# Kernel optimization log

Measured on AMD Instinct MI355X. Metric: run time of the kernel, lower is better.

## Reference

```python
import jax, jax.numpy as jnp
import numpy as np

N_NODES = 10000

def setup_inputs() -> dict:
    key = jax.random.key(0)
    k1, k2, k3, k4, k5 = jax.random.split(key, 5)
    n_edges = 640000
    d_in = 128
    d_out = 128
    x = jax.random.normal(k1, (N_NODES, d_in), dtype=jnp.float32)
    src = jax.random.randint(k2, (n_edges,), 0, N_NODES, dtype=jnp.int32)
    dst = jax.random.randint(k3, (n_edges,), 0, N_NODES, dtype=jnp.int32)
    W = jax.random.normal(k4, (d_in, d_out), dtype=jnp.float32) * (1.0 / np.sqrt(d_in))
    b = jax.random.normal(k5, (d_out,), dtype=jnp.float32) * 0.01
    return {"x": x, "src": src, "dst": dst, "W": W, "b": b}

def reference(x, src, dst, W, b):
    # copy_src + sum reduce: for each edge, send x[src]; each node sums incoming msgs
    msgs = x[src]  # [E, d_in] gather
    h = jax.ops.segment_sum(msgs, dst, num_segments=N_NODES)  # [N, d_in] scatter-add
    # dropout p=0.0 -> identity; linear + relu
    out = jax.nn.relu(h @ W + b)  # [N, d_out]
    return out
```

## Files before the change

kernel.cpp:

```cpp
#include <hip/hip_runtime.h>

#define N_NODES 10000
#define D 128
#define N_EDGES 640000
#define SHARDS 8
#define CPAD 16
#define BCAP 32
#define GEMM_BLOCKS 313
#define FILL_BLOCKS 625

__device__ __forceinline__ unsigned short f2bf(float f) {
  unsigned int u = __float_as_uint(f);
  unsigned int r = (u + 0x7fffu + ((u >> 16) & 1u)) >> 16;
  return (unsigned short)r;
}
__device__ __forceinline__ float bf2f(unsigned short s) {
  return __uint_as_float((unsigned int)s << 16);
}

__device__ __forceinline__ int cidx(int d, int sh) {
  return ((d << 3) | sh) << 4;
}

__global__ __launch_bounds__(256) void gcn_fused_kernel(
    const float* __restrict__ x, const float* __restrict__ W,
    unsigned short* __restrict__ xw,
    const int* __restrict__ src, const int* __restrict__ dst,
    int* __restrict__ counts, unsigned short* __restrict__ srcs_pad) {
  __shared__ unsigned short Wl[D * D];

  if (blockIdx.x < FILL_BLOCKS) {
    const int e4 = (blockIdx.x * 256 + threadIdx.x) * 4;
    const int sh = blockIdx.x & (SHARDS - 1);
    const int4 d4 = *(const int4*)(dst + e4);
    const int4 s4 = *(const int4*)(src + e4);

    int r0 = atomicAdd(&counts[cidx(d4.x, sh)], 1);
    int r1 = atomicAdd(&counts[cidx(d4.y, sh)], 1);
    int r2 = atomicAdd(&counts[cidx(d4.z, sh)], 1);
    int r3 = atomicAdd(&counts[cidx(d4.w, sh)], 1);
    if (r0 < BCAP) srcs_pad[((size_t)d4.x * SHARDS + sh) * BCAP + r0] = (unsigned short)s4.x;
    if (r1 < BCAP) srcs_pad[((size_t)d4.y * SHARDS + sh) * BCAP + r1] = (unsigned short)s4.y;
    if (r2 < BCAP) srcs_pad[((size_t)d4.z * SHARDS + sh) * BCAP + r2] = (unsigned short)s4.z;
    if (r3 < BCAP) srcs_pad[((size_t)d4.w * SHARDS + sh) * BCAP + r3] = (unsigned short)s4.w;
    return;
  }

  for (int i = threadIdx.x; i < D * D; i += 256) Wl[i] = f2bf(W[i]);
  __syncthreads();

  const int bid = blockIdx.x - FILL_BLOCKS;
  const int c0 = (threadIdx.x & 31) * 4;
  const int r0 = bid * 32 + (threadIdx.x >> 5) * 4;
  if (r0 >= N_NODES) return;

  float4 acc0 = {0, 0, 0, 0}, acc1 = acc0, acc2 = acc0, acc3 = acc0;
  const float* x0 = x + (size_t)r0 * D;

#define GEMM_STEP(J, HC)                                              \
  {                                                                   \
    ushort4 wu = *(const ushort4*)&Wl[(k4 + J) * D + c0];             \
    float wx = bf2f(wu.x), wy = bf2f(wu.y);                           \
    float wz = bf2f(wu.z), ww = bf2f(wu.w);                           \
    acc0.x = fmaf(hv0.HC, wx, acc0.x);                                \
    acc0.y = fmaf(hv0.HC, wy, acc0.y);                                \
    acc0.z = fmaf(hv0.HC, wz, acc0.z);                                \
    acc0.w = fmaf(hv0.HC, ww, acc0.w);                                \
    acc1.x = fmaf(hv1.HC, wx, acc1.x);                                \
    acc1.y = fmaf(hv1.HC, wy, acc1.y);                                \
    acc1.z = fmaf(hv1.HC, wz, acc1.z);                                \
    acc1.w = fmaf(hv1.HC, ww, acc1.w);                                \
    acc2.x = fmaf(hv2.HC, wx, acc2.x);                                \
    acc2.y = fmaf(hv2.HC, wy, acc2.y);                                \
    acc2.z = fmaf(hv2.HC, wz, acc2.z);                                \
    acc2.w = fmaf(hv2.HC, ww, acc2.w);                                \
    acc3.x = fmaf(hv3.HC, wx, acc3.x);                                \
    acc3.y = fmaf(hv3.HC, wy, acc3.y);                                \
    acc3.z = fmaf(hv3.HC, wz, acc3.z);                                \
    acc3.w = fmaf(hv3.HC, ww, acc3.w);                                \
  }

  for (int k4 = 0; k4 < D; k4 += 4) {
    float4 hv0 = *(const float4*)(x0 + 0 * D + k4);
    float4 hv1 = *(const float4*)(x0 + 1 * D + k4);
    float4 hv2 = *(const float4*)(x0 + 2 * D + k4);
    float4 hv3 = *(const float4*)(x0 + 3 * D + k4);
    GEMM_STEP(0, x)
    GEMM_STEP(1, y)
    GEMM_STEP(2, z)
    GEMM_STEP(3, w)
  }
#undef GEMM_STEP

  ushort4 sv;
#define STORE_ROW(R, ACC)                                              \
  sv.x = f2bf(ACC.x); sv.y = f2bf(ACC.y);                              \
  sv.z = f2bf(ACC.z); sv.w = f2bf(ACC.w);                              \
  *(ushort4*)(xw + (size_t)(r0 + R) * D + c0) = sv;
  STORE_ROW(0, acc0)
  STORE_ROW(1, acc1)
  STORE_ROW(2, acc2)
  STORE_ROW(3, acc3)
#undef STORE_ROW
}

__global__ __launch_bounds__(256) void gcn_gather_kernel(
    const unsigned short* __restrict__ xw, const int* __restrict__ counts,
    const unsigned short* __restrict__ srcs_pad,
    const float* __restrict__ b, float* __restrict__ out) {
  const int node = blockIdx.x * 4 + (threadIdx.x >> 6);
  const int lane = threadIdx.x & 63;

  int c = 0;
  if (lane < SHARDS) c = counts[cidx(node, lane)];

  const unsigned short* npad = srcs_pad + (size_t)node * (SHARDS * BCAP);
  const unsigned int* xw32 = (const unsigned int*)xw;
  float alo = 0.f, ahi = 0.f;

#pragma unroll
  for (int s = 0; s < SHARDS; ++s) {
    int len = __shfl(c, s, 64);
    if (len > BCAP) len = BCAP;
    int id = npad[s * BCAP + (lane & 31)];
    int j = 0;
    for (; j + 4 <= len; j += 4) {
      int sid0 = __shfl(id, j + 0, 64);
      int sid1 = __shfl(id, j + 1, 64);
      int sid2 = __shfl(id, j + 2, 64);
      int sid3 = __shfl(id, j + 3, 64);
      unsigned int u0 = xw32[sid0 * 64 + lane];
      unsigned int u1 = xw32[sid1 * 64 + lane];
      unsigned int u2 = xw32[sid2 * 64 + lane];
      unsigned int u3 = xw32[sid3 * 64 + lane];
      alo += __uint_as_float(u0 << 16);
      ahi += __uint_as_float(u0 & 0xffff0000u);
      alo += __uint_as_float(u1 << 16);
      ahi += __uint_as_float(u1 & 0xffff0000u);
      alo += __uint_as_float(u2 << 16);
      ahi += __uint_as_float(u2 & 0xffff0000u);
      alo += __uint_as_float(u3 << 16);
      ahi += __uint_as_float(u3 & 0xffff0000u);
    }
    if (j + 2 <= len) {
      int sid0 = __shfl(id, j + 0, 64);
      int sid1 = __shfl(id, j + 1, 64);
      unsigned int u0 = xw32[sid0 * 64 + lane];
      unsigned int u1 = xw32[sid1 * 64 + lane];
      alo += __uint_as_float(u0 << 16);
      ahi += __uint_as_float(u0 & 0xffff0000u);
      alo += __uint_as_float(u1 << 16);
      ahi += __uint_as_float(u1 & 0xffff0000u);
      j += 2;
    }
    if (j < len) {
      int sid = __shfl(id, j, 64);
      unsigned int u = xw32[sid * 64 + lane];
      alo += __uint_as_float(u << 16);
      ahi += __uint_as_float(u & 0xffff0000u);
    }
  }

  const float2 bv = *(const float2*)(b + lane * 2);
  float2 o;
  o.x = fmaxf(alo + bv.x, 0.f);
  o.y = fmaxf(ahi + bv.y, 0.f);
  *(float2*)(out + (size_t)node * D + lane * 2) = o;
}

extern "C" void kernel_launch(void* const* d_in, const int* in_sizes, int n_in,
                              void* d_out, int out_size, void* d_ws, size_t ws_size,
                              hipStream_t stream) {
  const float* x   = (const float*)d_in[0];
  const int*   src = (const int*)d_in[1];
  const int*   dst = (const int*)d_in[2];
  const float* W   = (const float*)d_in[3];
  const float* b   = (const float*)d_in[4];
  float* out = (float*)d_out;

  unsigned short* xw       = (unsigned short*)d_ws;
  int*            counts   = (int*)(xw + (size_t)N_NODES * D);
  unsigned short* srcs_pad = (unsigned short*)(counts + (size_t)N_NODES * SHARDS * CPAD);

  hipMemsetAsync(counts, 0, (size_t)N_NODES * SHARDS * CPAD * sizeof(int), stream);
  gcn_fused_kernel<<<FILL_BLOCKS + GEMM_BLOCKS, 256, 0, stream>>>(
      x, W, xw, src, dst, counts, srcs_pad);
  gcn_gather_kernel<<<N_NODES / 4, 256, 0, stream>>>(xw, counts, srcs_pad, b, out);
}
```

Measured before the change: 126.1 us.

## Gather four rows per wavefront with 16-byte loads and cross-group reduction

The gather kernel now splits each 64-lane wavefront into four 16-lane groups. Each group loads a whole bf16 row with uint4 (16-byte) loads, so four to eight neighbor rows are in flight per iteration instead of one row per instruction. All shard index lists are prefetched into registers up front, and partial sums are combined with xor shuffles before one group writes the output. This raises memory-level parallelism and load width, at the cost of more registers, a reduction step, and divergent tail predicates.

Result: faster. 120.6 us (-4.4%).

```diff
diff --git a/kernel.cpp b/kernel.cpp
--- a/kernel.cpp
+++ b/kernel.cpp
@@ -17,6 +17,8 @@
 __device__ __forceinline__ float bf2f(unsigned short s) {
   return __uint_as_float((unsigned int)s << 16);
 }
+__device__ __forceinline__ float blo(unsigned int u) { return __uint_as_float(u << 16); }
+__device__ __forceinline__ float bhi(unsigned int u) { return __uint_as_float(u & 0xffff0000u); }
 
 __device__ __forceinline__ int cidx(int d, int sh) {
   return ((d << 3) | sh) << 4;
@@ -110,62 +112,75 @@
     const float* __restrict__ b, float* __restrict__ out) {
   const int node = blockIdx.x * 4 + (threadIdx.x >> 6);
   const int lane = threadIdx.x & 63;
+  const int g = lane >> 4;
+  const int t = lane & 15;
 
   int c = 0;
   if (lane < SHARDS) c = counts[cidx(node, lane)];
 
   const unsigned short* npad = srcs_pad + (size_t)node * (SHARDS * BCAP);
+
+  int ids[SHARDS];
+#pragma unroll
+  for (int s = 0; s < SHARDS; ++s)
+    ids[s] = npad[s * BCAP + (lane & 31)];
+
   const unsigned int* xw32 = (const unsigned int*)xw;
-  float alo = 0.f, ahi = 0.f;
+  float a0 = 0.f, a1 = 0.f, a2 = 0.f, a3 = 0.f;
+  float a4 = 0.f, a5 = 0.f, a6 = 0.f, a7 = 0.f;
+
+#define ACC8(U)                                                        \
+  a0 += blo(U.x); a1 += bhi(U.x); a2 += blo(U.y); a3 += bhi(U.y);      \
+  a4 += blo(U.z); a5 += bhi(U.z); a6 += blo(U.w); a7 += bhi(U.w);
 
 #pragma unroll
   for (int s = 0; s < SHARDS; ++s) {
     int len = __shfl(c, s, 64);
     if (len > BCAP) len = BCAP;
-    int id = npad[s * BCAP + (lane & 31)];
-    int j = 0;
-    for (; j + 4 <= len; j += 4) {
-      int sid0 = __shfl(id, j + 0, 64);
-      int sid1 = __shfl(id, j + 1, 64);
-      int sid2 = __shfl(id, j + 2, 64);
-      int sid3 = __shfl(id, j + 3, 64);
-      unsigned int u0 = xw32[sid0 * 64 + lane];
-      unsigned int u1 = xw32[sid1 * 64 + lane];
-      unsigned int u2 = xw32[sid2 * 64 + lane];
-      unsigned int u3 = xw32[sid3 * 64 + lane];
-      alo += __uint_as_float(u0 << 16);
-      ahi += __uint_as_float(u0 & 0xffff0000u);
-      alo += __uint_as_float(u1 << 16);
-      ahi += __uint_as_float(u1 & 0xffff0000u);
-      alo += __uint_as_float(u2 << 16);
-      ahi += __uint_as_float(u2 & 0xffff0000u);
-      alo += __uint_as_float(u3 << 16);
-      ahi += __uint_as_float(u3 & 0xffff0000u);
+    const int id = ids[s];
+    for (int j = 0; j < len; j += 8) {
+      int sidA = __shfl(id, j + g, 64);
+      int sidB = __shfl(id, j + 4 + g, 64);
+      if (j + g < len) {
+        uint4 u = *(const uint4*)(xw32 + (size_t)sidA * 64 + t * 4);
+        ACC8(u)
+      }
+      if (j + 4 + g < len) {
+        uint4 u = *(const uint4*)(xw32 + (size_t)sidB * 64 + t * 4);
+        ACC8(u)
+      }
     }
-    if (j + 2 <= len) {
-      int sid0 = __shfl(id, j + 0, 64);
-      int sid1 = __shfl(id, j + 1, 64);
-      unsigned int u0 = xw32[sid0 * 64 + lane];
-      unsigned int u1 = xw32[sid1 * 64 + lane];
-      alo += __uint_as_float(u0 << 16);
-      ahi += __uint_as_float(u0 & 0xffff0000u);
-      alo += __uint_as_float(u1 << 16);
-      ahi += __uint_as_float(u1 & 0xffff0000u);
-      j += 2;
-    }
-    if (j < len) {
-      int sid = __shfl(id, j, 64);
-      unsigned int u = xw32[sid * 64 + lane];
-      alo += __uint_as_float(u << 16);
-      ahi += __uint_as_float(u & 0xffff0000u);
-    }
-  }
-
-  const float2 bv = *(const float2*)(b + lane * 2);
-  float2 o;
-  o.x = fmaxf(alo + bv.x, 0.f);
-  o.y = fmaxf(ahi + bv.y, 0.f);
-  *(float2*)(out + (size_t)node * D + lane * 2) = o;
+  }
+#undef ACC8
+
+#pragma unroll
+  for (int d = 16; d <= 32; d <<= 1) {
+    a0 += __shfl_xor(a0, d, 64);
+    a1 += __shfl_xor(a1, d, 64);
+    a2 += __shfl_xor(a2, d, 64);
+    a3 += __shfl_xor(a3, d, 64);
+    a4 += __shfl_xor(a4, d, 64);
+    a5 += __shfl_xor(a5, d, 64);
+    a6 += __shfl_xor(a6, d, 64);
+    a7 += __shfl_xor(a7, d, 64);
+  }
+
+  if (g == 0) {
+    const float4 b0 = *(const float4*)(b + t * 8);
+    const float4 b1 = *(const float4*)(b + t * 8 + 4);
+    float4 o0, o1;
+    o0.x = fmaxf(a0 + b0.x, 0.f);
+    o0.y = fmaxf(a1 + b0.y, 0.f);
+    o0.z = fmaxf(a2 + b0.z, 0.f);
+    o0.w = fmaxf(a3 + b0.w, 0.f);
+    o1.x = fmaxf(a4 + b1.x, 0.f);
+    o1.y = fmaxf(a5 + b1.y, 0.f);
+    o1.z = fmaxf(a6 + b1.z, 0.f);
+    o1.w = fmaxf(a7 + b1.w, 0.f);
+    float* op = out + (size_t)node * D + t * 8;
+    *(float4*)op = o0;
+    *(float4*)(op + 4) = o1;
+  }
 }
 
 extern "C" void kernel_launch(void* const* d_in, const int* in_sizes, int n_in,
```
